# Performance work log

Measured on AMD Instinct MI355X. Metric: run time of the kernel, lower is better.

## Reference

```python
import jax, jax.numpy as jnp
import numpy as np

IN_DIM = 2
OUT_DIM = 3  # number of independent CScalar heads (u, v, p)
HID = 16
N = 4194304


def setup_inputs() -> dict:
    key = jax.random.key(0)
    ks = jax.random.split(key, 7)
    s1 = 1.0 / np.sqrt(IN_DIM)
    s2 = 1.0 / np.sqrt(HID)
    x = jax.random.normal(ks[0], (N, IN_DIM), dtype=jnp.float32)
    # Stacked parameters for the OUT_DIM independent tiny MLPs
    W1 = jax.random.uniform(ks[1], (OUT_DIM, IN_DIM, HID), jnp.float32, -s1, s1)
    b1 = jax.random.uniform(ks[2], (OUT_DIM, HID), jnp.float32, -s1, s1)
    W2 = jax.random.uniform(ks[3], (OUT_DIM, HID, HID), jnp.float32, -s2, s2)
    b2 = jax.random.uniform(ks[4], (OUT_DIM, HID), jnp.float32, -s2, s2)
    W3 = jax.random.uniform(ks[5], (OUT_DIM, HID), jnp.float32, -s2, s2)  # last layer HID->1, squeezed
    b3 = jax.random.uniform(ks[6], (OUT_DIM,), jnp.float32, -s2, s2)
    return {"x": x, "W1": W1, "b1": b1, "W2": W2, "b2": b2, "W3": W3, "b3": b3}


def reference(x, W1, b1, W2, b2, W3, b3):
    # All OUT_DIM tiny MLPs batched as one grouped GEMM chain.
    # h1: [E, N, H]
    h1 = jax.nn.relu(jnp.einsum('ni,eih->enh', x, W1) + b1[:, None, :])
    h2 = jax.nn.relu(jnp.einsum('enh,ehk->enk', h1, W2) + b2[:, None, :])
    y = jnp.einsum('enh,eh->en', h2, W3) + b3[:, None]  # [E, N]
    return y.T  # [N, E] == torch.hstack of per-head [N,1] outputs
```

## Files before the change

### kernel.cpp

```cpp
#include <hip/hip_runtime.h>
#include <hip/hip_bf16.h>

typedef __attribute__((ext_vector_type(2)))  float f32x2;
typedef __attribute__((ext_vector_type(8)))  float f32x8;
typedef __attribute__((ext_vector_type(16))) float f32x16;
typedef __attribute__((ext_vector_type(2)))  __bf16 bf16x2;
typedef __attribute__((ext_vector_type(8)))  __bf16 bf16x8;
typedef __attribute__((ext_vector_type(4)))  unsigned int u32x4;

static __device__ __forceinline__ bf16x8 cvt8(f32x8 v) {
    return __builtin_convertvector(v, bf16x8);
}
static __device__ __forceinline__ unsigned int pkcvt(f32x2 v) {
    return __builtin_bit_cast(unsigned int, __builtin_convertvector(v, bf16x2));
}
static __device__ __forceinline__ f32x2 max2(f32x2 v) {
    const f32x2 z = {0.f, 0.f};
    return __builtin_elementwise_max(v, z);
}

#define MFMA32(A, B, C) __builtin_amdgcn_mfma_f32_32x32x16_bf16((A), (B), (C), 0, 0, 0)

__global__ __launch_bounds__(256, 3) void mlp3_mfma32(
    const float* __restrict__ x,
    const float* __restrict__ W1, const float* __restrict__ b1,
    const float* __restrict__ W2, const float* __restrict__ b2,
    const float* __restrict__ W3, const float* __restrict__ b3,
    float* __restrict__ out, int n)
{
    const int tid  = (int)threadIdx.x;
    const int lane = tid & 63;
    const int row  = lane & 31;
    const int h    = lane >> 5;
    const int wv   = tid >> 6;

    bf16x8 a1[3], a2[3];
    f32x2  w3p[3][4], b2p[3][4];
    #pragma unroll
    for (int e = 0; e < 3; ++e) {
        f32x8 t = {0.f,0.f,0.f,0.f,0.f,0.f,0.f,0.f};
        if (h == 0 && row < 16) {
            t[0] = W1[e * 32 + row];
            t[1] = W1[e * 32 + 16 + row];
            t[2] = b1[e * 16 + row];
        }
        a1[e] = cvt8(t);
        f32x8 t2 = {0.f,0.f,0.f,0.f,0.f,0.f,0.f,0.f};
        if (row < 16) {
            #pragma unroll
            for (int i = 0; i < 8; ++i) {
                const int k = (i & 3) + 8 * (i >> 2) + 4 * h;
                t2[i] = W2[e * 256 + k * 16 + row];
            }
        }
        a2[e] = cvt8(t2);
        #pragma unroll
        for (int j = 0; j < 4; ++j) {
            const int i0 = 2 * j, i1 = 2 * j + 1;
            const int k0 = (i0 & 3) + 8 * (i0 >> 2) + 4 * h;
            const int k1 = (i1 & 3) + 8 * (i1 >> 2) + 4 * h;
            w3p[e][j] = (f32x2){ W3[e * 16 + k0], W3[e * 16 + k1] };
            b2p[e][j] = (f32x2){ b2[e * 16 + k0], b2[e * 16 + k1] };
        }
    }
    const float b30 = b3[0], b31 = b3[1], b32 = b3[2];
    f32x16 zz;
    #pragma unroll
    for (int r = 0; r < 16; ++r) zz[r] = 0.f;

    const int xoff = (wv * 32 + row) * 8;
    const int ooff = (wv * 32 + row) * 12;

    const int nblk   = n >> 7;
    const int stride = (int)gridDim.x;

    int cb = (int)blockIdx.x;
    float2 xv = *reinterpret_cast<const float2*>((const char*)x + (size_t)cb * 1024 + xoff);

    while (true) {
        const int nb = cb + stride;
        const bool more = nb < nblk;
        float2 xn;
        if (more)
            xn = *reinterpret_cast<const float2*>((const char*)x + (size_t)nb * 1024 + xoff);

        u32x4 bu = { pkcvt((f32x2){xv.x, xv.y}), 0x3F80u, 0u, 0u };
        const bf16x8 bx = __builtin_bit_cast(bf16x8, bu);

        float ys[3];
        #pragma unroll
        for (int e = 0; e < 3; ++e) {
            f32x16 t1 = MFMA32(a1[e], bx, zz);
            u32x4 bhw;
            #pragma unroll
            for (int j = 0; j < 4; ++j)
                bhw[j] = pkcvt(max2((f32x2){ t1[2*j], t1[2*j+1] }));
            const bf16x8 bh = __builtin_bit_cast(bf16x8, bhw);

            f32x16 t2 = MFMA32(a2[e], bh, zz);
            f32x2 yp = {0.f, 0.f};
            #pragma unroll
            for (int j = 0; j < 4; ++j) {
                f32x2 q = max2((f32x2){ t2[2*j], t2[2*j+1] } + b2p[e][j]);
                yp += w3p[e][j] * q;
            }
            const float ysum = yp[0] + yp[1];
            ys[e] = ysum + __shfl_xor(ysum, 32, 64);
        }

        if (lane < 32) {
            *reinterpret_cast<float3*>((char*)out + (size_t)cb * 1536 + ooff) =
                make_float3(ys[0] + b30, ys[1] + b31, ys[2] + b32);
        }

        if (!more) break;
        cb = nb;
        xv = xn;
    }
}

extern "C" void kernel_launch(void* const* d_in, const int* in_sizes, int n_in,
                              void* d_out, int out_size, void* d_ws, size_t ws_size,
                              hipStream_t stream) {
    const float* x  = (const float*)d_in[0];
    const float* W1 = (const float*)d_in[1];
    const float* b1 = (const float*)d_in[2];
    const float* W2 = (const float*)d_in[3];
    const float* b2 = (const float*)d_in[4];
    const float* W3 = (const float*)d_in[5];
    const float* b3 = (const float*)d_in[6];
    float* out = (float*)d_out;
    (void)d_ws; (void)ws_size; (void)n_in; (void)out_size;

    const int n = in_sizes[0] / 2;
    const int block = 256;
    const int grid = 2048;

    mlp3_mfma32<<<grid, block, 0, stream>>>(x, W1, b1, W2, b2, W3, b3, out, n);
}
```

Baseline: 51.44 us.

## Pack two heads into one layer-1 MFMA and compute final layer via MFMA

Layer 1 now packs heads 0 and 1 into a single 32-row MFMA, with a second MFMA for head 2, so three layer-1 MFMAs become two. The final HID->1 dot product moves from scalar FMAs plus a cross-lane shuffle to an MFMA that accumulates all three heads into one output tile. b2 is stored packed as bf16 to save registers, and launch bounds rise to 4 blocks per SIMD. In exchange it adds an extra bf16 rounding of the layer-2 activations and of W3/b2, which lowers accuracy, and it spends MFMA issue slots on a mostly empty 32x32 tile.

```diff
diff --git a/kernel.cpp b/kernel.cpp
--- a/kernel.cpp
+++ b/kernel.cpp
@@ -18,10 +18,16 @@
     const f32x2 z = {0.f, 0.f};
     return __builtin_elementwise_max(v, z);
 }
+static __device__ __forceinline__ f32x2 bfexp(unsigned int u) {
+    f32x2 r;
+    r[0] = __builtin_bit_cast(float, u << 16);
+    r[1] = __builtin_bit_cast(float, u & 0xFFFF0000u);
+    return r;
+}
 
 #define MFMA32(A, B, C) __builtin_amdgcn_mfma_f32_32x32x16_bf16((A), (B), (C), 0, 0, 0)
 
-__global__ __launch_bounds__(256, 3) void mlp3_mfma32(
+__global__ __launch_bounds__(256, 4) void mlp3_mfma32(
     const float* __restrict__ x,
     const float* __restrict__ W1, const float* __restrict__ b1,
     const float* __restrict__ W2, const float* __restrict__ b2,
@@ -34,33 +40,51 @@
     const int h    = lane >> 5;
     const int wv   = tid >> 6;
 
-    bf16x8 a1[3], a2[3];
-    f32x2  w3p[3][4], b2p[3][4];
+    bf16x8 a1d, a1s;
+    {
+        f32x8 t = {0.f,0.f,0.f,0.f,0.f,0.f,0.f,0.f};
+        if (h == 0) {
+            const int hd = row >> 4, j = row & 15;
+            t[0] = W1[hd * 32 + j];
+            t[1] = W1[hd * 32 + 16 + j];
+            t[2] = b1[hd * 16 + j];
+        }
+        a1d = cvt8(t);
+        f32x8 s = {0.f,0.f,0.f,0.f,0.f,0.f,0.f,0.f};
+        if (h == 0 && row < 16) {
+            s[0] = W1[64 + row];
+            s[1] = W1[80 + row];
+            s[2] = b1[32 + row];
+        }
+        a1s = cvt8(s);
+    }
+    bf16x8 a2[3], a3[3];
+    u32x4  b2pk[3];
     #pragma unroll
     for (int e = 0; e < 3; ++e) {
-        f32x8 t = {0.f,0.f,0.f,0.f,0.f,0.f,0.f,0.f};
-        if (h == 0 && row < 16) {
-            t[0] = W1[e * 32 + row];
-            t[1] = W1[e * 32 + 16 + row];
-            t[2] = b1[e * 16 + row];
-        }
-        a1[e] = cvt8(t);
-        f32x8 t2 = {0.f,0.f,0.f,0.f,0.f,0.f,0.f,0.f};
+        f32x8 t2v = {0.f,0.f,0.f,0.f,0.f,0.f,0.f,0.f};
         if (row < 16) {
             #pragma unroll
             for (int i = 0; i < 8; ++i) {
                 const int k = (i & 3) + 8 * (i >> 2) + 4 * h;
-                t2[i] = W2[e * 256 + k * 16 + row];
+                t2v[i] = W2[e * 256 + k * 16 + row];
             }
         }
-        a2[e] = cvt8(t2);
+        a2[e] = cvt8(t2v);
+        f32x8 t3 = {0.f,0.f,0.f,0.f,0.f,0.f,0.f,0.f};
+        if (row == e) {
+            #pragma unroll
+            for (int i = 0; i < 8; ++i) {
+                const int k = (i & 3) + 8 * (i >> 2) + 4 * h;
+                t3[i] = W3[e * 16 + k];
+            }
+        }
+        a3[e] = cvt8(t3);
         #pragma unroll
         for (int j = 0; j < 4; ++j) {
-            const int i0 = 2 * j, i1 = 2 * j + 1;
-            const int k0 = (i0 & 3) + 8 * (i0 >> 2) + 4 * h;
-            const int k1 = (i1 & 3) + 8 * (i1 >> 2) + 4 * h;
-            w3p[e][j] = (f32x2){ W3[e * 16 + k0], W3[e * 16 + k1] };
-            b2p[e][j] = (f32x2){ b2[e * 16 + k0], b2[e * 16 + k1] };
+            const int k0 = ((2*j) & 3) + 8 * ((2*j) >> 2) + 4 * h;
+            const int k1 = ((2*j+1) & 3) + 8 * ((2*j+1) >> 2) + 4 * h;
+            b2pk[e][j] = pkcvt((f32x2){ b2[e * 16 + k0], b2[e * 16 + k1] });
         }
     }
     const float b30 = b3[0], b31 = b3[1], b32 = b3[2];
@@ -87,30 +111,37 @@
         u32x4 bu = { pkcvt((f32x2){xv.x, xv.y}), 0x3F80u, 0u, 0u };
         const bf16x8 bx = __builtin_bit_cast(bf16x8, bu);
 
-        float ys[3];
+        f32x16 t1d = MFMA32(a1d, bx, zz);
+        f32x16 t1s = MFMA32(a1s, bx, zz);
+        u32x4 w0, w1, w2;
+        #pragma unroll
+        for (int j = 0; j < 4; ++j) {
+            w0[j] = pkcvt(max2((f32x2){ t1d[2*j],     t1d[2*j + 1] }));
+            w1[j] = pkcvt(max2((f32x2){ t1d[8 + 2*j], t1d[8 + 2*j + 1] }));
+            w2[j] = pkcvt(max2((f32x2){ t1s[2*j],     t1s[2*j + 1] }));
+        }
+        const bf16x8 bh0 = __builtin_bit_cast(bf16x8, w0);
+        const bf16x8 bh1 = __builtin_bit_cast(bf16x8, w1);
+        const bf16x8 bh2 = __builtin_bit_cast(bf16x8, w2);
+
+        f32x16 y;
         #pragma unroll
         for (int e = 0; e < 3; ++e) {
-            f32x16 t1 = MFMA32(a1[e], bx, zz);
-            u32x4 bhw;
-            #pragma unroll
-            for (int j = 0; j < 4; ++j)
-                bhw[j] = pkcvt(max2((f32x2){ t1[2*j], t1[2*j+1] }));
-            const bf16x8 bh = __builtin_bit_cast(bf16x8, bhw);
-
+            const bf16x8 bh = (e == 0) ? bh0 : ((e == 1) ? bh1 : bh2);
             f32x16 t2 = MFMA32(a2[e], bh, zz);
-            f32x2 yp = {0.f, 0.f};
+            u32x4 bw;
             #pragma unroll
             for (int j = 0; j < 4; ++j) {
-                f32x2 q = max2((f32x2){ t2[2*j], t2[2*j+1] } + b2p[e][j]);
-                yp += w3p[e][j] * q;
+                f32x2 q = (f32x2){ t2[2*j], t2[2*j + 1] } + bfexp(b2pk[e][j]);
+                bw[j] = pkcvt(max2(q));
             }
-            const float ysum = yp[0] + yp[1];
-            ys[e] = ysum + __shfl_xor(ysum, 32, 64);
+            const bf16x8 bt = __builtin_bit_cast(bf16x8, bw);
+            y = MFMA32(a3[e], bt, (e == 0) ? zz : y);
         }
 
         if (lane < 32) {
             *reinterpret_cast<float3*>((char*)out + (size_t)cb * 1536 + ooff) =
-                make_float3(ys[0] + b30, ys[1] + b31, ys[2] + b32);
+                make_float3(y[0] + b30, y[1] + b31, y[2] + b32);
         }
 
         if (!more) break;
```

New measurement: 50.46 us. No clear change (-1.9%).

## Switch to 16x16x32 MFMA with layer-3 and biases folded into MFMA

Applied to the files above, without the earlier changes.

Replaces the 32x32x16 MFMA path with 16x16x32 MFMAs. Each wave now handles its 32 rows as two 16-row tiles, which removes the wasted half of the 32-wide tiles. The b2 bias goes into the MFMA accumulator, and the final HID->1 layer for all three heads runs as an accumulated MFMA seeded with b3. This replaces the scalar FMA reduction and the cross-lane shuffle. Output stores are deferred by one iteration to overlap with the next tile's compute, and occupancy hint rises to 4. The risks are more MFMA issues per tile, an extra bf16 rounding on the layer-3 input, and higher register pressure under the tighter launch bound.

```diff
diff --git a/kernel.cpp b/kernel.cpp
--- a/kernel.cpp
+++ b/kernel.cpp
@@ -2,8 +2,8 @@
 #include <hip/hip_bf16.h>
 
 typedef __attribute__((ext_vector_type(2)))  float f32x2;
+typedef __attribute__((ext_vector_type(4)))  float f32x4;
 typedef __attribute__((ext_vector_type(8)))  float f32x8;
-typedef __attribute__((ext_vector_type(16))) float f32x16;
 typedef __attribute__((ext_vector_type(2)))  __bf16 bf16x2;
 typedef __attribute__((ext_vector_type(8)))  __bf16 bf16x8;
 typedef __attribute__((ext_vector_type(4)))  unsigned int u32x4;
@@ -19,9 +19,9 @@
     return __builtin_elementwise_max(v, z);
 }
 
-#define MFMA32(A, B, C) __builtin_amdgcn_mfma_f32_32x32x16_bf16((A), (B), (C), 0, 0, 0)
+#define MFMA16(A, B, C) __builtin_amdgcn_mfma_f32_16x16x32_bf16((A), (B), (C), 0, 0, 0)
 
-__global__ __launch_bounds__(256, 3) void mlp3_mfma32(
+__global__ __launch_bounds__(256, 4) void mlp3_mfma16(
     const float* __restrict__ x,
     const float* __restrict__ W1, const float* __restrict__ b1,
     const float* __restrict__ W2, const float* __restrict__ b2,
@@ -30,92 +30,109 @@
 {
     const int tid  = (int)threadIdx.x;
     const int lane = tid & 63;
-    const int row  = lane & 31;
-    const int h    = lane >> 5;
+    const int col  = lane & 15;
+    const int g    = lane >> 4;
     const int wv   = tid >> 6;
 
-    bf16x8 a1[3], a2[3];
-    f32x2  w3p[3][4], b2p[3][4];
+    bf16x8 a1[3], a2[3], a3[3];
+    f32x4  c2[3];
     #pragma unroll
     for (int e = 0; e < 3; ++e) {
         f32x8 t = {0.f,0.f,0.f,0.f,0.f,0.f,0.f,0.f};
-        if (h == 0 && row < 16) {
-            t[0] = W1[e * 32 + row];
-            t[1] = W1[e * 32 + 16 + row];
-            t[2] = b1[e * 16 + row];
+        if (g == 0) {
+            t[0] = W1[e * 32 + col];
+            t[1] = W1[e * 32 + 16 + col];
+            t[2] = b1[e * 16 + col];
         }
         a1[e] = cvt8(t);
         f32x8 t2 = {0.f,0.f,0.f,0.f,0.f,0.f,0.f,0.f};
-        if (row < 16) {
+        #pragma unroll
+        for (int i = 0; i < 4; ++i)
+            t2[i] = W2[e * 256 + (4 * g + i) * 16 + col];
+        a2[e] = cvt8(t2);
+        f32x8 t3 = {0.f,0.f,0.f,0.f,0.f,0.f,0.f,0.f};
+        if (col == e) {
             #pragma unroll
-            for (int i = 0; i < 8; ++i) {
-                const int k = (i & 3) + 8 * (i >> 2) + 4 * h;
-                t2[i] = W2[e * 256 + k * 16 + row];
-            }
+            for (int i = 0; i < 4; ++i)
+                t3[i] = W3[e * 16 + 4 * g + i];
         }
-        a2[e] = cvt8(t2);
+        a3[e] = cvt8(t3);
         #pragma unroll
-        for (int j = 0; j < 4; ++j) {
-            const int i0 = 2 * j, i1 = 2 * j + 1;
-            const int k0 = (i0 & 3) + 8 * (i0 >> 2) + 4 * h;
-            const int k1 = (i1 & 3) + 8 * (i1 >> 2) + 4 * h;
-            w3p[e][j] = (f32x2){ W3[e * 16 + k0], W3[e * 16 + k1] };
-            b2p[e][j] = (f32x2){ b2[e * 16 + k0], b2[e * 16 + k1] };
-        }
+        for (int r = 0; r < 4; ++r)
+            c2[e][r] = b2[e * 16 + 4 * g + r];
     }
-    const float b30 = b3[0], b31 = b3[1], b32 = b3[2];
-    f32x16 zz;
-    #pragma unroll
-    for (int r = 0; r < 16; ++r) zz[r] = 0.f;
+    f32x4 c30 = {0.f, 0.f, 0.f, 0.f};
+    if (g == 0) { c30[0] = b3[0]; c30[1] = b3[1]; c30[2] = b3[2]; }
+    const f32x4 zz = {0.f, 0.f, 0.f, 0.f};
 
-    const int xoff = (wv * 32 + row) * 8;
-    const int ooff = (wv * 32 + row) * 12;
+    const int xoff = (wv * 32 + col) * 8;
+    const int ooff = (wv * 32 + col) * 12;
 
     const int nblk   = n >> 7;
     const int stride = (int)gridDim.x;
+    const size_t xstep = (size_t)stride * 1024;
+    const size_t ostep = (size_t)stride * 1536;
 
     int cb = (int)blockIdx.x;
-    float2 xv = *reinterpret_cast<const float2*>((const char*)x + (size_t)cb * 1024 + xoff);
+    const char* xp = (const char*)x + (size_t)cb * 1024 + xoff;
+    char*       op = (char*)out + (size_t)cb * 1536 + ooff;
+
+    float2 xv0 = *reinterpret_cast<const float2*>(xp);
+    float2 xv1 = *reinterpret_cast<const float2*>(xp + 128);
+
+    f32x4 y0, y1;
+    char* paddr = nullptr;
+    bool  pendv = false;
 
     while (true) {
-        const int nb = cb + stride;
-        const bool more = nb < nblk;
-        float2 xn;
-        if (more)
-            xn = *reinterpret_cast<const float2*>((const char*)x + (size_t)nb * 1024 + xoff);
+        const bool more = (cb + stride) < nblk;
+        float2 xn0, xn1;
+        if (more) {
+            xn0 = *reinterpret_cast<const float2*>(xp + xstep);
+            xn1 = *reinterpret_cast<const float2*>(xp + xstep + 128);
+        }
 
-        u32x4 bu = { pkcvt((f32x2){xv.x, xv.y}), 0x3F80u, 0u, 0u };
-        const bf16x8 bx = __builtin_bit_cast(bf16x8, bu);
+        if (pendv && lane < 16) {
+            *reinterpret_cast<float3*>(paddr)       = make_float3(y0[0], y0[1], y0[2]);
+            *reinterpret_cast<float3*>(paddr + 192) = make_float3(y1[0], y1[1], y1[2]);
+        }
 
-        float ys[3];
+        u32x4 bu0 = { pkcvt((f32x2){xv0.x, xv0.y}), 0x3F80u, 0u, 0u };
+        u32x4 bu1 = { pkcvt((f32x2){xv1.x, xv1.y}), 0x3F80u, 0u, 0u };
+        const bf16x8 bx0 = __builtin_bit_cast(bf16x8, bu0);
+        const bf16x8 bx1 = __builtin_bit_cast(bf16x8, bu1);
+
         #pragma unroll
         for (int e = 0; e < 3; ++e) {
-            f32x16 t1 = MFMA32(a1[e], bx, zz);
-            u32x4 bhw;
-            #pragma unroll
-            for (int j = 0; j < 4; ++j)
-                bhw[j] = pkcvt(max2((f32x2){ t1[2*j], t1[2*j+1] }));
-            const bf16x8 bh = __builtin_bit_cast(bf16x8, bhw);
-
-            f32x16 t2 = MFMA32(a2[e], bh, zz);
-            f32x2 yp = {0.f, 0.f};
-            #pragma unroll
-            for (int j = 0; j < 4; ++j) {
-                f32x2 q = max2((f32x2){ t2[2*j], t2[2*j+1] } + b2p[e][j]);
-                yp += w3p[e][j] * q;
-            }
-            const float ysum = yp[0] + yp[1];
-            ys[e] = ysum + __shfl_xor(ysum, 32, 64);
+            f32x4 t10 = MFMA16(a1[e], bx0, zz);
+            f32x4 t11 = MFMA16(a1[e], bx1, zz);
+            u32x4 w0 = { pkcvt(max2((f32x2){t10[0], t10[1]})),
+                         pkcvt(max2((f32x2){t10[2], t10[3]})), 0u, 0u };
+            u32x4 w1 = { pkcvt(max2((f32x2){t11[0], t11[1]})),
+                         pkcvt(max2((f32x2){t11[2], t11[3]})), 0u, 0u };
+            f32x4 t20 = MFMA16(a2[e], __builtin_bit_cast(bf16x8, w0), c2[e]);
+            f32x4 t21 = MFMA16(a2[e], __builtin_bit_cast(bf16x8, w1), c2[e]);
+            u32x4 v0 = { pkcvt(max2((f32x2){t20[0], t20[1]})),
+                         pkcvt(max2((f32x2){t20[2], t20[3]})), 0u, 0u };
+            u32x4 v1 = { pkcvt(max2((f32x2){t21[0], t21[1]})),
+                         pkcvt(max2((f32x2){t21[2], t21[3]})), 0u, 0u };
+            y0 = MFMA16(a3[e], __builtin_bit_cast(bf16x8, v0), (e == 0) ? c30 : y0);
+            y1 = MFMA16(a3[e], __builtin_bit_cast(bf16x8, v1), (e == 0) ? c30 : y1);
         }
 
-        if (lane < 32) {
-            *reinterpret_cast<float3*>((char*)out + (size_t)cb * 1536 + ooff) =
-                make_float3(ys[0] + b30, ys[1] + b31, ys[2] + b32);
-        }
+        paddr = op;
+        pendv = true;
 
         if (!more) break;
-        cb = nb;
-        xv = xn;
+        cb += stride;
+        xp += xstep;
+        op += ostep;
+        xv0 = xn0; xv1 = xn1;
+    }
+
+    if (pendv && lane < 16) {
+        *reinterpret_cast<float3*>(paddr)       = make_float3(y0[0], y0[1], y0[2]);
+        *reinterpret_cast<float3*>(paddr + 192) = make_float3(y1[0], y1[1], y1[2]);
     }
 }
 
@@ -136,5 +153,5 @@
     const int block = 256;
     const int grid = 2048;
 
-    mlp3_mfma32<<<grid, block, 0, stream>>>(x, W1, b1, W2, b2, W3, b3, out, n);
+    mlp3_mfma16<<<grid, block, 0, stream>>>(x, W1, b1, W2, b2, W3, b3, out, n);
 }
```

Measured after the change: 52.20 us. About the same (+1.5%).
